# Optimization experiments

Hardware: AMD Instinct MI355X
Metric: run time of the kernel (lower is better)

## Reference

```python
import jax, jax.numpy as jnp
import numpy as np
import math

B, S, L, H, NH, FF, V = 32, 512, 12, 768, 12, 3072, 30522
DH = H // NH


def setup_inputs() -> dict:
    key = jax.random.key(0)
    ks = jax.random.split(key, 16)
    w = lambda k, shape: (jax.random.normal(k, shape, jnp.float32) * 0.02)
    return {
        "input_ids": jax.random.randint(ks[0], (B, S), 0, V, dtype=jnp.int32),
        "attention_mask": jax.random.uniform(ks[1], (B, S), jnp.float32),
        "word_emb": w(ks[2], (V, H)),
        "pos_emb": w(ks[3], (S, H)),
        "type_emb": w(ks[4], (H,)),
        "ln_emb_s": jnp.ones((H,), jnp.float32),
        "ln_emb_b": jnp.zeros((H,), jnp.float32),
        "Wq": w(ks[5], (L, H, H)), "bq": jnp.zeros((L, H), jnp.float32),
        "Wk": w(ks[6], (L, H, H)), "bk": jnp.zeros((L, H), jnp.float32),
        "Wv": w(ks[7], (L, H, H)), "bv": jnp.zeros((L, H), jnp.float32),
        "Wo": w(ks[8], (L, H, H)), "bo": jnp.zeros((L, H), jnp.float32),
        "ln1_s": jnp.ones((L, H), jnp.float32), "ln1_b": jnp.zeros((L, H), jnp.float32),
        "Wi": w(ks[9], (L, H, FF)), "bi": jnp.zeros((L, FF), jnp.float32),
        "Wf": w(ks[10], (L, FF, H)), "bf": jnp.zeros((L, H), jnp.float32),
        "ln2_s": jnp.ones((L, H), jnp.float32), "ln2_b": jnp.zeros((L, H), jnp.float32),
    }


def _ln(x, s, b):
    # BERT LayerNorm, eps=1e-12
    m = jnp.mean(x, -1, keepdims=True)
    v = jnp.mean((x - m) ** 2, -1, keepdims=True)
    return (x - m) * jax.lax.rsqrt(v + 1e-12) * s + b


def reference(input_ids, attention_mask, word_emb, pos_emb, type_emb,
              ln_emb_s, ln_emb_b, Wq, bq, Wk, bk, Wv, bv, Wo, bo,
              ln1_s, ln1_b, Wi, bi, Wf, bf, ln2_s, ln2_b):
    b, s = input_ids.shape
    scale = 1.0 / math.sqrt(DH)
    # Embeddings: word + position + (single) token-type, then LayerNorm
    h = word_emb[input_ids] + pos_emb[None, :s] + type_emb
    h = _ln(h, ln_emb_s, ln_emb_b)
    key_mask = attention_mask[:, None, None, :]  # [B,1,1,S], float

    def layer(h, p):
        wq, bq_, wk, bk_, wv, bv_, wo, bo_, l1s, l1b, wi, bi_, wf, bf_, l2s, l2b = p
        q = (jnp.einsum('bsd,de->bse', h, wq) + bq_).reshape(b, s, NH, DH)
        k = (jnp.einsum('bsd,de->bse', h, wk) + bk_).reshape(b, s, NH, DH)
        v = (jnp.einsum('bsd,de->bse', h, wv) + bv_).reshape(b, s, NH, DH)
        scores = jnp.einsum('bqhd,bkhd->bhqk', q, k) * scale
        probs = jax.nn.softmax(scores, axis=-1)
        # post-softmax masking + renormalization (the non-standard part)
        probs = probs * key_mask
        probs = probs / jnp.clip(jnp.sum(probs, -1, keepdims=True), 1e-9, None)
        ctx = jnp.einsum('bhqk,bkhd->bqhd', probs, v).reshape(b, s, H)
        attn_out = _ln(jnp.einsum('bsd,de->bse', ctx, wo) + bo_ + h, l1s, l1b)
        inter = jax.nn.gelu(jnp.einsum('bsd,df->bsf', attn_out, wi) + bi_, approximate=False)
        out = _ln(jnp.einsum('bsf,fd->bsd', inter, wf) + bf_ + attn_out, l2s, l2b)
        return out, None

    h, _ = jax.lax.scan(layer, h, (Wq, bq, Wk, bk, Wv, bv, Wo, bo,
                                   ln1_s, ln1_b, Wi, bi, Wf, bf, ln2_s, ln2_b))
    # masked mean pooling + L2 normalize (normalize=True)
    m = attention_mask[..., None]
    sent = jnp.sum(h * m, axis=1) / jnp.clip(jnp.sum(m, axis=1), 1e-6, None)
    sent = sent / jnp.clip(jnp.linalg.norm(sent, axis=-1, keepdims=True), 1e-12, None)
    return sent
```

## Files before the change

### kernel.cpp

```cpp
#include <hip/hip_runtime.h>
#include <hip/hip_bf16.h>
#include <math.h>

typedef __bf16 bf16;
typedef __bf16 bf16x8 __attribute__((ext_vector_type(8)));
typedef float  f32x4  __attribute__((ext_vector_type(4)));

#define B_  32
#define S_  512
#define H_  768
#define NH_ 12
#define DH_ 64
#define FF_ 3072
#define L_  12
#define M_  (B_*S_)
#define QKV_ 2304

#define KST 68
#define VST 516
#define PST 68

__device__ __forceinline__ void gload16(const bf16* g, bf16* l) {
  __builtin_amdgcn_global_load_lds(
      (const __attribute__((address_space(1))) void*)g,
      (__attribute__((address_space(3))) void*)l, 16, 0, 0);
}

__device__ __forceinline__ float fast_gelu(float x) {
  float z = x * 0.70710678118f;
  float s = fabsf(z);
  float t = __builtin_amdgcn_rcpf(1.0f + 0.3275911f * s);
  float p = t*(0.254829592f + t*(-0.284496736f + t*(1.421413741f +
            t*(-1.453152027f + t*1.061405429f))));
  float e = p * __expf(-s*s);
  float erfv = copysignf(1.0f - e, z);
  return 0.5f * x * (1.0f + erfv);
}

__global__ __launch_bounds__(512, 4) void gemm128(
    const bf16* __restrict__ A, const bf16* __restrict__ Bt,
    const float* __restrict__ bias, void* __restrict__ outp,
    int N, int K, int tiles_n, int epi)
{
  __shared__ bf16 As[128*64];
  __shared__ bf16 Bs[128*64];
  const int tid  = threadIdx.x;
  const int lane = tid & 63, wid = tid >> 6;
  const int wr = wid >> 2, wc = wid & 3;
  const int lrow = lane & 15, kgrp = lane >> 4;

  const int nwg = gridDim.x, orig = blockIdx.x;
  const int qc = nwg >> 3, rc = nwg & 7;
  const int xcd = orig & 7, lin = orig >> 3;
  const int wg = (xcd < rc ? xcd*(qc+1) : rc*(qc+1) + (xcd-rc)*qc) + lin;
  const int tm = wg / tiles_n, tn = wg % tiles_n;
  const size_t m0 = (size_t)tm * 128, n0 = (size_t)tn * 128;
  const int KT = K >> 6;

  const bf16* Ab = A  + m0 * K;
  const bf16* Bb = Bt + n0 * K;

  auto stage = [&](const bf16* gbase, bf16* ldsbase, int kt) {
#pragma unroll
    for (int j = 0; j < 2; ++j) {
      int lin2  = j*512 + tid;
      int prow  = lin2 >> 3;
      int pslot = lin2 & 7;
      int lslot = pslot ^ (prow & 7);
      const bf16* src = gbase + (size_t)prow * K + (size_t)kt*64 + lslot*8;
      bf16* dst = ldsbase + (size_t)(j*512 + (wid<<6))*8;
      gload16(src, dst);
    }
  };

  f32x4 acc[4][2] = {};

  for (int t = 0; t < KT; ++t) {
    __syncthreads();
    stage(Ab, As, t);
    stage(Bb, Bs, t);
    __syncthreads();
#pragma unroll
    for (int kk = 0; kk < 2; ++kk) {
      bf16x8 a[4], b[2];
#pragma unroll
      for (int m = 0; m < 4; ++m) {
        int row  = wr*64 + m*16 + lrow;
        int slot = (kk*4 + kgrp) ^ (lrow & 7);
        a[m] = *(const bf16x8*)&As[row*64 + slot*8];
      }
#pragma unroll
      for (int n = 0; n < 2; ++n) {
        int row  = wc*32 + n*16 + lrow;
        int slot = (kk*4 + kgrp) ^ (lrow & 7);
        b[n] = *(const bf16x8*)&Bs[row*64 + slot*8];
      }
#pragma unroll
      for (int m = 0; m < 4; ++m)
#pragma unroll
        for (int n = 0; n < 2; ++n)
          acc[m][n] = __builtin_amdgcn_mfma_f32_16x16x32_bf16(a[m], b[n], acc[m][n], 0, 0, 0);
    }
  }

#pragma unroll
  for (int m = 0; m < 4; ++m)
#pragma unroll
    for (int n = 0; n < 2; ++n) {
      int col = (int)n0 + wc*32 + n*16 + lrow;
      float bv = bias[col];
#pragma unroll
      for (int r = 0; r < 4; ++r) {
        int row = (int)m0 + wr*64 + m*16 + kgrp*4 + r;
        float x = acc[m][n][r] + bv;
        size_t idx = (size_t)row * N + col;
        if (epi == 1)      ((float*)outp)[idx] = x;
        else if (epi == 0) ((bf16*)outp)[idx]  = (bf16)x;
        else               ((bf16*)outp)[idx]  = (bf16)fast_gelu(x);
      }
    }
}

__global__ __launch_bounds__(256) void weight_prep(
    const float* __restrict__ Wq, const float* __restrict__ Wk,
    const float* __restrict__ Wv, const float* __restrict__ Wo,
    const float* __restrict__ Wi, const float* __restrict__ Wf,
    const float* __restrict__ bq, const float* __restrict__ bk,
    const float* __restrict__ bv,
    bf16* __restrict__ wqkv, bf16* __restrict__ wot,
    bf16* __restrict__ wit,  bf16* __restrict__ wft,
    float* __restrict__ qkbias)
{
  int bid = blockIdx.x;
  if (bid >= 1728) {
    int i = (bid - 1728)*256 + threadIdx.x;
    if (i < QKV_)
      qkbias[i] = (i < 768) ? bq[i] : (i < 1536 ? bk[i-768] : bv[i-1536]);
    return;
  }
  const float* W; bf16* Wt; int K, N, t;
  if (bid < 576) {
    K = 768; N = 768;
    if      (bid < 144) { W = Wq; Wt = wqkv;             t = bid; }
    else if (bid < 288) { W = Wk; Wt = wqkv + 768*768;   t = bid - 144; }
    else if (bid < 432) { W = Wv; Wt = wqkv + 2*768*768; t = bid - 288; }
    else                { W = Wo; Wt = wot;              t = bid - 432; }
  } else if (bid < 1152) { W = Wi; Wt = wit; K = 768;  N = 3072; t = bid - 576; }
  else                   { W = Wf; Wt = wft; K = 3072; N = 768;  t = bid - 1152; }
  const int kt = K >> 6;
  const int k0 = (t % kt)*64, n0 = (t / kt)*64;

  __shared__ bf16 T[64][65];
  int tx = threadIdx.x & 63, ty = threadIdx.x >> 6;
#pragma unroll
  for (int j = 0; j < 16; ++j) {
    int kk = j*4 + ty;
    T[kk][tx] = (bf16)W[(size_t)(k0+kk)*N + n0 + tx];
  }
  __syncthreads();
#pragma unroll
  for (int j = 0; j < 16; ++j) {
    int nn = j*4 + ty;
    Wt[(size_t)(n0+nn)*K + k0 + tx] = T[tx][nn];
  }
}

__device__ __forceinline__ void block_sum2(float& a, float& b, float* red) {
  int lane = threadIdx.x & 63, wid = threadIdx.x >> 6;
  for (int o = 32; o > 0; o >>= 1) { a += __shfl_xor(a, o); b += __shfl_xor(b, o); }
  if (lane == 0) { red[wid*2] = a; red[wid*2+1] = b; }
  __syncthreads();
  a = red[0] + red[2] + red[4] + red[6];
  b = red[1] + red[3] + red[5] + red[7];
  __syncthreads();
}

__global__ __launch_bounds__(256) void embed_ln(
    const int* __restrict__ ids, const float* __restrict__ we,
    const float* __restrict__ pe, const float* __restrict__ te,
    const float* __restrict__ gs, const float* __restrict__ gb,
    float* __restrict__ h32, bf16* __restrict__ hb)
{
  __shared__ float red[8];
  int row = blockIdx.x;
  int s = row & (S_-1);
  int id = ids[row];
  int t = threadIdx.x;
  float x[3], sum = 0.f, sq = 0.f;
#pragma unroll
  for (int j = 0; j < 3; ++j) {
    int c = t + j*256;
    float v = we[(size_t)id*H_ + c] + pe[(size_t)s*H_ + c] + te[c];
    x[j] = v; sum += v; sq += v*v;
  }
  block_sum2(sum, sq, red);
  float mean = sum * (1.f/H_);
  float var  = sq  * (1.f/H_) - mean*mean;
  float rstd = rsqrtf(fmaxf(var, 0.f) + 1e-12f);
#pragma unroll
  for (int j = 0; j < 3; ++j) {
    int c = t + j*256;
    float y = (x[j]-mean)*rstd*gs[c] + gb[c];
    h32[(size_t)row*H_ + c] = y;
    hb [(size_t)row*H_ + c] = (bf16)y;
  }
}

__global__ __launch_bounds__(256) void ln_res(
    const float* __restrict__ t32, const float* __restrict__ res,
    const float* __restrict__ gs, const float* __restrict__ gb,
    float* __restrict__ o32, bf16* __restrict__ ob)
{
  __shared__ float red[8];
  int row = blockIdx.x, t = threadIdx.x;
  float x[3], sum = 0.f, sq = 0.f;
#pragma unroll
  for (int j = 0; j < 3; ++j) {
    int c = t + j*256;
    float v = t32[(size_t)row*H_ + c] + res[(size_t)row*H_ + c];
    x[j] = v; sum += v; sq += v*v;
  }
  block_sum2(sum, sq, red);
  float mean = sum * (1.f/H_);
  float var  = sq  * (1.f/H_) - mean*mean;
  float rstd = rsqrtf(fmaxf(var, 0.f) + 1e-12f);
#pragma unroll
  for (int j = 0; j < 3; ++j) {
    int c = t + j*256;
    float y = (x[j]-mean)*rstd*gs[c] + gb[c];
    o32[(size_t)row*H_ + c] = y;
    ob [(size_t)row*H_ + c] = (bf16)y;
  }
}

__global__ __launch_bounds__(512, 2) void attn_kernel(
    const bf16* __restrict__ qkv, const float* __restrict__ mask,
    bf16* __restrict__ ctx)
{
  __shared__ bf16 Kl[S_*KST];
  __shared__ bf16 Vt[DH_*VST];
  __shared__ float mk[S_];
  __shared__ bf16 Pl[8][16*PST];
  int tid = threadIdx.x, lane = tid & 63, wid = tid >> 6;
  int lrow = lane & 15, kgrp = lane >> 4;
  int cur_head = -1;

  for (int u = 0; u < 6; ++u) {
    int unit = blockIdx.x*6 + u;
    int hh = unit >> 2, pass = unit & 3;
    int b = hh / NH_, h = hh % NH_;
    const bf16* Qb = qkv + (size_t)(b*S_)*QKV_ + h*DH_;

    if (hh != cur_head) {
      __syncthreads();
      const bf16* Kb = qkv + (size_t)(b*S_)*QKV_ + H_   + h*DH_;
      const bf16* Vb = qkv + (size_t)(b*S_)*QKV_ + 2*H_ + h*DH_;
      for (int it = 0; it < 8; ++it) {
        int slot = it*512 + tid;
        int s = slot >> 3, c8 = (slot & 7)*8;
        bf16x8 kv = *(const bf16x8*)&Kb[(size_t)s*QKV_ + c8];
#pragma unroll
        for (int i = 0; i < 8; ++i) kv[i] = (bf16)((float)kv[i] * 0.125f);
        *(bf16x8*)&Kl[s*KST + c8] = kv;
        bf16x8 v = *(const bf16x8*)&Vb[(size_t)s*QKV_ + c8];
#pragma unroll
        for (int i = 0; i < 8; ++i) Vt[(c8+i)*VST + s] = v[i];
      }
      mk[tid] = mask[b*S_ + tid];
      cur_head = hh;
      __syncthreads();
    }

    int q0 = pass*128 + wid*16;
    bf16x8 qa[2];
#pragma unroll
    for (int kc = 0; kc < 2; ++kc)
      qa[kc] = *(const bf16x8*)&Qb[(size_t)(q0 + lrow)*QKV_ + kc*32 + kgrp*8];
    f32x4 O[4] = {};
    float mrun[4], lrun[4];
#pragma unroll
    for (int r = 0; r < 4; ++r) { mrun[r] = -1e30f; lrun[r] = 0.f; }

    for (int c0 = 0; c0 < S_; c0 += 64) {
      f32x4 Sf[4] = {};
      __builtin_amdgcn_s_setprio(1);
#pragma unroll
      for (int kc = 0; kc < 2; ++kc)
#pragma unroll
        for (int sn = 0; sn < 4; ++sn) {
          bf16x8 kbv = *(const bf16x8*)&Kl[(c0 + sn*16 + lrow)*KST + kc*32 + kgrp*8];
          Sf[sn] = __builtin_amdgcn_mfma_f32_16x16x32_bf16(qa[kc], kbv, Sf[sn], 0, 0, 0);
        }
      __builtin_amdgcn_s_setprio(0);
      float cmax[4];
#pragma unroll
      for (int r = 0; r < 4; ++r) cmax[r] = -1e30f;
#pragma unroll
      for (int sn = 0; sn < 4; ++sn)
#pragma unroll
        for (int r = 0; r < 4; ++r)
          cmax[r] = fmaxf(cmax[r], Sf[sn][r]);
      for (int o = 1; o < 16; o <<= 1)
#pragma unroll
        for (int r = 0; r < 4; ++r) cmax[r] = fmaxf(cmax[r], __shfl_xor(cmax[r], o));

      bool small = (cmax[0] <= mrun[0]+8.f) && (cmax[1] <= mrun[1]+8.f) &&
                   (cmax[2] <= mrun[2]+8.f) && (cmax[3] <= mrun[3]+8.f);
      bool skip = __all(small);
      float newm[4], fr[4], lsum[4];
      if (skip) {
#pragma unroll
        for (int r = 0; r < 4; ++r) { newm[r] = mrun[r]; fr[r] = 1.f; lsum[r] = 0.f; }
      } else {
#pragma unroll
        for (int r = 0; r < 4; ++r) {
          newm[r] = fmaxf(mrun[r], cmax[r]);
          fr[r]   = __expf(mrun[r] - newm[r]);
          lsum[r] = 0.f;
        }
      }
#pragma unroll
      for (int sn = 0; sn < 4; ++sn) {
        float mkv = mk[c0 + sn*16 + lrow];
#pragma unroll
        for (int r = 0; r < 4; ++r) {
          float e = __expf(Sf[sn][r] - newm[r]) * mkv;
          bf16 eb = (bf16)e;
          lsum[r] += (float)eb;
          Pl[wid][(kgrp*4 + r)*PST + sn*16 + lrow] = eb;
        }
      }
      if (!skip) {
#pragma unroll
        for (int on = 0; on < 4; ++on)
#pragma unroll
          for (int r = 0; r < 4; ++r) O[on][r] *= fr[r];
      }
      asm volatile("s_waitcnt lgkmcnt(0)" ::: "memory");
      __builtin_amdgcn_sched_barrier(0);
      __builtin_amdgcn_s_setprio(1);
#pragma unroll
      for (int kc = 0; kc < 2; ++kc) {
        bf16x8 pa = *(const bf16x8*)&Pl[wid][lrow*PST + kc*32 + kgrp*8];
#pragma unroll
        for (int on = 0; on < 4; ++on) {
          bf16x8 vv = *(const bf16x8*)&Vt[(on*16 + lrow)*VST + c0 + kc*32 + kgrp*8];
          O[on] = __builtin_amdgcn_mfma_f32_16x16x32_bf16(pa, vv, O[on], 0, 0, 0);
        }
      }
      __builtin_amdgcn_s_setprio(0);
      for (int o = 1; o < 16; o <<= 1)
#pragma unroll
        for (int r = 0; r < 4; ++r) lsum[r] += __shfl_xor(lsum[r], o);
#pragma unroll
      for (int r = 0; r < 4; ++r) { lrun[r] = lrun[r]*fr[r] + lsum[r]; mrun[r] = newm[r]; }
    }
#pragma unroll
    for (int on = 0; on < 4; ++on)
#pragma unroll
      for (int r = 0; r < 4; ++r) {
        float val = O[on][r] / fmaxf(lrun[r], 1e-9f);
        int q = q0 + kgrp*4 + r;
        ctx[(size_t)(b*S_ + q)*H_ + h*DH_ + on*16 + lrow] = (bf16)val;
      }
  }
}

__global__ __launch_bounds__(256) void pool_norm(
    const float* __restrict__ h32, const float* __restrict__ mask,
    float* __restrict__ out)
{
  __shared__ float red[8];
  int b = blockIdx.x, t = threadIdx.x;
  float a0 = 0.f, a1 = 0.f, a2 = 0.f;
  for (int s = 0; s < S_; ++s) {
    float m = mask[b*S_ + s];
    const float* hp = &h32[((size_t)b*S_ + s)*H_];
    a0 += hp[t]*m; a1 += hp[t+256]*m; a2 += hp[t+512]*m;
  }
  float msum = mask[b*S_ + t] + mask[b*S_ + 256 + t];
  float dummy = 0.f;
  block_sum2(msum, dummy, red);
  float inv = 1.f / fmaxf(msum, 1e-6f);
  float s0 = a0*inv, s1 = a1*inv, s2 = a2*inv;
  float nrm = s0*s0 + s1*s1 + s2*s2;
  dummy = 0.f;
  block_sum2(nrm, dummy, red);
  float rn = 1.f / fmaxf(sqrtf(nrm), 1e-12f);
  out[b*H_ + t]       = s0*rn;
  out[b*H_ + t + 256] = s1*rn;
  out[b*H_ + t + 512] = s2*rn;
}

extern "C" void kernel_launch(void* const* d_in, const int* in_sizes, int n_in,
                              void* d_out, int out_size, void* d_ws, size_t ws_size,
                              hipStream_t stream)
{
  const int*   ids  = (const int*)  d_in[0];
  const float* mask = (const float*)d_in[1];
  const float* we   = (const float*)d_in[2];
  const float* pe   = (const float*)d_in[3];
  const float* te   = (const float*)d_in[4];
  const float* les  = (const float*)d_in[5];
  const float* leb  = (const float*)d_in[6];
  const float* Wq   = (const float*)d_in[7];
  const float* bq   = (const float*)d_in[8];
  const float* Wk   = (const float*)d_in[9];
  const float* bk   = (const float*)d_in[10];
  const float* Wv   = (const float*)d_in[11];
  const float* bv   = (const float*)d_in[12];
  const float* Wo   = (const float*)d_in[13];
  const float* bo   = (const float*)d_in[14];
  const float* l1s  = (const float*)d_in[15];
  const float* l1b  = (const float*)d_in[16];
  const float* Wi   = (const float*)d_in[17];
  const float* bi   = (const float*)d_in[18];
  const float* Wf   = (const float*)d_in[19];
  const float* bfp  = (const float*)d_in[20];
  const float* l2s  = (const float*)d_in[21];
  const float* l2b  = (const float*)d_in[22];

  char* p = (char*)d_ws;
  auto alloc = [&](size_t bytes) { char* q = p; p += (bytes + 255) & ~(size_t)255; return q; };
  bf16*  wqkv = (bf16*) alloc((size_t)QKV_*H_*2);
  bf16*  wot  = (bf16*) alloc((size_t)H_*H_*2);
  bf16*  wit  = (bf16*) alloc((size_t)H_*FF_*2);
  bf16*  wft  = (bf16*) alloc((size_t)H_*FF_*2);
  float* qkbias=(float*)alloc((size_t)QKV_*4);
  bf16*  hb   = (bf16*) alloc((size_t)M_*H_*2);
  float* h32  = (float*)alloc((size_t)M_*H_*4);
  float* a32  = (float*)alloc((size_t)M_*H_*4);
  float* tmp  = (float*)alloc((size_t)M_*H_*4);
  bf16*  qkvb = (bf16*) alloc((size_t)M_*QKV_*2);
  bf16*  cxb  = (bf16*) alloc((size_t)M_*H_*2);
  bf16*  inb  = (bf16*) alloc((size_t)M_*FF_*2);

  embed_ln<<<M_, 256, 0, stream>>>(ids, we, pe, te, les, leb, h32, hb);

  for (int l = 0; l < L_; ++l) {
    size_t wsq = (size_t)l*H_*H_;
    weight_prep<<<1737, 256, 0, stream>>>(
        Wq + wsq, Wk + wsq, Wv + wsq, Wo + wsq,
        Wi + (size_t)l*H_*FF_, Wf + (size_t)l*FF_*H_,
        bq + l*H_, bk + l*H_, bv + l*H_,
        wqkv, wot, wit, wft, qkbias);

    gemm128<<<128*(QKV_/128), 512, 0, stream>>>(hb,  wqkv, qkbias,      qkvb, QKV_, H_,  QKV_/128, 0);
    attn_kernel<<<256, 512, 0, stream>>>(qkvb, mask, cxb);
    gemm128<<<128*(H_/128),  512, 0, stream>>>(cxb, wot, bo  + l*H_,  tmp,  H_,  H_,  H_/128,  1);
    ln_res<<<M_, 256, 0, stream>>>(tmp, h32, l1s + l*H_, l1b + l*H_, a32, hb);
    gemm128<<<128*(FF_/128), 512, 0, stream>>>(hb,  wit, bi  + l*FF_, inb,  FF_, H_,  FF_/128, 2);
    gemm128<<<128*(H_/128),  512, 0, stream>>>(inb, wft, bfp + l*H_,  tmp,  H_,  FF_, H_/128,  1);
    ln_res<<<M_, 256, 0, stream>>>(tmp, a32, l2s + l*H_, l2b + l*H_, h32, hb);
  }

  pool_norm<<<B_, 256, 0, stream>>>(h32, mask, (float*)d_out);
}
```

Baseline: 5.475 ms.

## Load attention K tile via direct-to-LDS swizzled loads and split pooling

The K tile for each head is now loaded straight from global memory into LDS with global_load_lds, using an XOR-swizzled unpadded layout in place of padding to avoid bank conflicts. Because the loaded K can no longer be pre-scaled, the 1/sqrt(d) scaling moves to the Q fragments held in registers. The final masked mean pooling is also split into a partial-sum kernel over 256 blocks plus a small finalize kernel, which adds parallelism to what was a 32-block tail. Scaling Q instead of K changes bf16 rounding slightly. There is also no explicit wait between the async LDS load and the barrier, which could be a correctness risk depending on how the compiler handles waitcnt.

Measured after the change: 5.383 ms. No clear change (-1.7%).

```diff
diff --git a/kernel.cpp b/kernel.cpp
--- a/kernel.cpp
+++ b/kernel.cpp
@@ -16,7 +16,6 @@
 #define M_  (B_*S_)
 #define QKV_ 2304
 
-#define KST 68
 #define VST 516
 #define PST 68
 
@@ -237,7 +236,7 @@
     const bf16* __restrict__ qkv, const float* __restrict__ mask,
     bf16* __restrict__ ctx)
 {
-  __shared__ bf16 Kl[S_*KST];
+  __shared__ bf16 Kl[S_*64];
   __shared__ bf16 Vt[DH_*VST];
   __shared__ float mk[S_];
   __shared__ bf16 Pl[8][16*PST];
@@ -255,13 +254,18 @@
       __syncthreads();
       const bf16* Kb = qkv + (size_t)(b*S_)*QKV_ + H_   + h*DH_;
       const bf16* Vb = qkv + (size_t)(b*S_)*QKV_ + 2*H_ + h*DH_;
+#pragma unroll
+      for (int it = 0; it < 8; ++it) {
+        int lin   = it*512 + tid;
+        int prow  = lin >> 3;
+        int pslot = lin & 7;
+        int lslot = pslot ^ (prow & 7);
+        gload16(&Kb[(size_t)prow*QKV_ + lslot*8],
+                &Kl[(size_t)(it*512 + (wid<<6))*8]);
+      }
       for (int it = 0; it < 8; ++it) {
         int slot = it*512 + tid;
         int s = slot >> 3, c8 = (slot & 7)*8;
-        bf16x8 kv = *(const bf16x8*)&Kb[(size_t)s*QKV_ + c8];
-#pragma unroll
-        for (int i = 0; i < 8; ++i) kv[i] = (bf16)((float)kv[i] * 0.125f);
-        *(bf16x8*)&Kl[s*KST + c8] = kv;
         bf16x8 v = *(const bf16x8*)&Vb[(size_t)s*QKV_ + c8];
 #pragma unroll
         for (int i = 0; i < 8; ++i) Vt[(c8+i)*VST + s] = v[i];
@@ -274,8 +278,12 @@
     int q0 = pass*128 + wid*16;
     bf16x8 qa[2];
 #pragma unroll
-    for (int kc = 0; kc < 2; ++kc)
+    for (int kc = 0; kc < 2; ++kc) {
       qa[kc] = *(const bf16x8*)&Qb[(size_t)(q0 + lrow)*QKV_ + kc*32 + kgrp*8];
+#pragma unroll
+      for (int i = 0; i < 8; ++i)
+        qa[kc][i] = (bf16)((float)qa[kc][i] * 0.125f);
+    }
     f32x4 O[4] = {};
     float mrun[4], lrun[4];
 #pragma unroll
@@ -288,7 +296,9 @@
       for (int kc = 0; kc < 2; ++kc)
 #pragma unroll
         for (int sn = 0; sn < 4; ++sn) {
-          bf16x8 kbv = *(const bf16x8*)&Kl[(c0 + sn*16 + lrow)*KST + kc*32 + kgrp*8];
+          int row  = c0 + sn*16 + lrow;
+          int slot = (kc*4 + kgrp) ^ (lrow & 7);
+          bf16x8 kbv = *(const bf16x8*)&Kl[(size_t)row*64 + slot*8];
           Sf[sn] = __builtin_amdgcn_mfma_f32_16x16x32_bf16(qa[kc], kbv, Sf[sn], 0, 0, 0);
         }
       __builtin_amdgcn_s_setprio(0);
@@ -366,23 +376,39 @@
   }
 }
 
-__global__ __launch_bounds__(256) void pool_norm(
+__global__ __launch_bounds__(256) void pool_partial(
     const float* __restrict__ h32, const float* __restrict__ mask,
-    float* __restrict__ out)
-{
-  __shared__ float red[8];
-  int b = blockIdx.x, t = threadIdx.x;
+    float* __restrict__ part)
+{
+  int b = blockIdx.x >> 3, ch = blockIdx.x & 7;
+  int t = threadIdx.x;
   float a0 = 0.f, a1 = 0.f, a2 = 0.f;
-  for (int s = 0; s < S_; ++s) {
+  for (int s = ch*64; s < ch*64 + 64; ++s) {
     float m = mask[b*S_ + s];
     const float* hp = &h32[((size_t)b*S_ + s)*H_];
     a0 += hp[t]*m; a1 += hp[t+256]*m; a2 += hp[t+512]*m;
+  }
+  float* pp = &part[(size_t)(b*8 + ch)*H_];
+  pp[t] = a0; pp[t+256] = a1; pp[t+512] = a2;
+}
+
+__global__ __launch_bounds__(256) void pool_final(
+    const float* __restrict__ part, const float* __restrict__ mask,
+    float* __restrict__ out)
+{
+  __shared__ float red[8];
+  int b = blockIdx.x, t = threadIdx.x;
+  float s0 = 0.f, s1 = 0.f, s2 = 0.f;
+#pragma unroll
+  for (int ch = 0; ch < 8; ++ch) {
+    const float* pp = &part[(size_t)(b*8 + ch)*H_];
+    s0 += pp[t]; s1 += pp[t+256]; s2 += pp[t+512];
   }
   float msum = mask[b*S_ + t] + mask[b*S_ + 256 + t];
   float dummy = 0.f;
   block_sum2(msum, dummy, red);
   float inv = 1.f / fmaxf(msum, 1e-6f);
-  float s0 = a0*inv, s1 = a1*inv, s2 = a2*inv;
+  s0 *= inv; s1 *= inv; s2 *= inv;
   float nrm = s0*s0 + s1*s1 + s2*s2;
   dummy = 0.f;
   block_sum2(nrm, dummy, red);
@@ -434,6 +460,7 @@
   bf16*  qkvb = (bf16*) alloc((size_t)M_*QKV_*2);
   bf16*  cxb  = (bf16*) alloc((size_t)M_*H_*2);
   bf16*  inb  = (bf16*) alloc((size_t)M_*FF_*2);
+  float* part = (float*)alloc((size_t)B_*8*H_*4);
 
   embed_ln<<<M_, 256, 0, stream>>>(ids, we, pe, te, les, leb, h32, hb);
 
@@ -454,5 +481,6 @@
     ln_res<<<M_, 256, 0, stream>>>(tmp, a32, l2s + l*H_, l2b + l*H_, h32, hb);
   }
 
-  pool_norm<<<B_, 256, 0, stream>>>(h32, mask, (float*)d_out);
-}
+  pool_partial<<<B_*8, 256, 0, stream>>>(h32, mask, part);
+  pool_final<<<B_, 256, 0, stream>>>(part, mask, (float*)d_out);
+}
```
